# Kernel optimization log

Hardware: AMD Instinct MI355X
Metric: run time of the kernel (lower is better)

Reference implementation:

```python
import jax, jax.numpy as jnp
import numpy as np

B, S, D, H, DK, DV, DFF, L, V = 8, 1024, 256, 8, 32, 32, 1024, 4, 28
EPS = 1e-5
NEG = -1e9


def _ln(x, w, b):
    m = jnp.mean(x, axis=-1, keepdims=True)
    v = jnp.var(x, axis=-1, keepdims=True)
    return (x - m) * jax.lax.rsqrt(v + EPS) * w + b


def setup_inputs() -> dict:
    key = jax.random.key(0)
    ks = jax.random.split(key, 30)
    std = 0.02
    inp = {
        'input_ids': jax.random.randint(ks[0], (B, S), 0, V),
        'tok_embed': jax.random.normal(ks[1], (V, D), jnp.float32) * std,
        'pos_embed': jax.random.normal(ks[2], (S, D), jnp.float32) * std,
        'emb_ln_w': jnp.ones((D,), jnp.float32),
        'emb_ln_b': jnp.zeros((D,), jnp.float32),
        'Wq': jax.random.normal(ks[3], (L, D, H * DK), jnp.float32) * std,
        'bq': jnp.zeros((L, H * DK), jnp.float32),
        'Wk': jax.random.normal(ks[4], (L, D, H * DK), jnp.float32) * std,
        'bk': jnp.zeros((L, H * DK), jnp.float32),
        'Wv': jax.random.normal(ks[5], (L, D, H * DV), jnp.float32) * std,
        'bv': jnp.zeros((L, H * DV), jnp.float32),
        'Wo': jax.random.normal(ks[6], (L, H * DV, D), jnp.float32) * std,
        'bo': jnp.zeros((L, D), jnp.float32),
        'ln_w': jnp.ones((L, D), jnp.float32),
        'ln_b': jnp.zeros((L, D), jnp.float32),
        'W1': jax.random.normal(ks[7], (L, D, DFF), jnp.float32) * std,
        'b1': jnp.zeros((L, DFF), jnp.float32),
        'W2': jax.random.normal(ks[8], (L, DFF, D), jnp.float32) * std,
        'b2': jnp.zeros((L, D), jnp.float32),
        'ft1_w': jax.random.normal(ks[9], (D, D), jnp.float32) * std,
        'ft1_b': jnp.zeros((D,), jnp.float32),
        'ft2_w': jax.random.normal(ks[10], (D, D // 2), jnp.float32) * std,
        'ft2_b': jnp.zeros((D // 2,), jnp.float32),
        'cls_w': jax.random.normal(ks[11], (D // 2, 2), jnp.float32) * std,
        'cls_b': jnp.zeros((2,), jnp.float32),
    }
    return inp


def reference(input_ids, tok_embed, pos_embed, emb_ln_w, emb_ln_b,
              Wq, bq, Wk, bk, Wv, bv, Wo, bo, ln_w, ln_b,
              W1, b1, W2, b2, ft1_w, ft1_b, ft2_w, ft2_b, cls_w, cls_b):
    # Embedding: tok + pos, then LayerNorm
    x = tok_embed[input_ids] + pos_embed[jnp.arange(S)][None, :, :]
    x = _ln(x, emb_ln_w, emb_ln_b)
    # pad mask: True where key position is pad (token id 0); broadcast [B,1,1,S]
    pad = (input_ids == 0)[:, None, None, :]
    scale = 1.0 / np.sqrt(DK)
    for i in range(L):
        residual = x
        q = (x @ Wq[i] + bq[i]).reshape(B, S, H, DK).transpose(0, 2, 1, 3)
        k = (x @ Wk[i] + bk[i]).reshape(B, S, H, DK).transpose(0, 2, 1, 3)
        v = (x @ Wv[i] + bv[i]).reshape(B, S, H, DV).transpose(0, 2, 1, 3)
        scores = jnp.einsum('bhqd,bhkd->bhqk', q, k) * scale
        scores = jnp.where(pad, NEG, scores)
        attn = jax.nn.softmax(scores, axis=-1)
        ctx = jnp.einsum('bhqk,bhkd->bhqd', attn, v)
        ctx = ctx.transpose(0, 2, 1, 3).reshape(B, S, H * DV)
        x = _ln(ctx @ Wo[i] + bo[i] + residual, ln_w[i], ln_b[i])
        # FFN (note: original has NO residual/norm after FFN)
        x = jax.nn.relu(x @ W1[i] + b1[i]) @ W2[i] + b2[i]
    cls = x[:, 0, :]
    feat = jax.nn.relu(cls @ ft1_w + ft1_b) @ ft2_w + ft2_b  # dropout = eval no-op
    logits = feat @ cls_w + cls_b
    return logits, feat
```

## Files before the change

### kernel.cpp

```cpp
#include <hip/hip_runtime.h>
#include <math.h>

#define S_ 1024
#define D_ 256

typedef __attribute__((ext_vector_type(8))) _Float16 half8;
typedef __attribute__((ext_vector_type(4))) _Float16 half4;
typedef __attribute__((ext_vector_type(4))) float f32x4;
typedef __attribute__((ext_vector_type(4))) unsigned int u32x4;

__device__ __forceinline__ float wave_sum64(float x) {
    x += __shfl_xor(x, 32); x += __shfl_xor(x, 16); x += __shfl_xor(x, 8);
    x += __shfl_xor(x, 4);  x += __shfl_xor(x, 2);  x += __shfl_xor(x, 1);
    return x;
}

__device__ __forceinline__ unsigned int pk2h(float lo, float hi) {
    unsigned short a = __builtin_bit_cast(unsigned short, (_Float16)lo);
    unsigned short b = __builtin_bit_cast(unsigned short, (_Float16)hi);
    return (unsigned int)a | ((unsigned int)b << 16);
}

#define GLD16(gp, lp) __builtin_amdgcn_global_load_lds( \
    (const __attribute__((address_space(1))) void*)(gp), \
    (__attribute__((address_space(3))) void*)(lp), 16, 0, 0)

__global__ __launch_bounds__(256) void transpose_cvt(
    const float* __restrict__ src, _Float16* __restrict__ dst, int K, int N)
{
    __shared__ float tile[32][33];
    src += (size_t)blockIdx.z * K * N;
    dst += (size_t)blockIdx.z * K * N;
    const int bx = blockIdx.x * 32;
    const int by = blockIdx.y * 32;
    const int t = threadIdx.x;
    const int c = t & 31, r0 = t >> 5;
    #pragma unroll
    for (int j = 0; j < 4; ++j)
        tile[r0 + 8 * j][c] = src[(size_t)(by + r0 + 8 * j) * N + bx + c];
    __syncthreads();
    #pragma unroll
    for (int j = 0; j < 4; ++j)
        dst[(size_t)(bx + r0 + 8 * j) * K + by + c] = (_Float16)tile[c][r0 + 8 * j];
}

__global__ __launch_bounds__(256) void transpose_qkv(
    const float* __restrict__ Wq, const float* __restrict__ Wk,
    const float* __restrict__ Wv, _Float16* __restrict__ qkvT)
{
    __shared__ float tile[32][33];
    const int z = blockIdx.z, l = z / 3, m = z % 3;
    const float* src = (m == 0 ? Wq : (m == 1 ? Wk : Wv)) + (size_t)l * 65536;
    _Float16* dst = qkvT + (size_t)l * 196608 + (size_t)m * 65536;
    const int bx = blockIdx.x * 32;
    const int by = blockIdx.y * 32;
    const int t = threadIdx.x;
    const int c = t & 31, r0 = t >> 5;
    #pragma unroll
    for (int j = 0; j < 4; ++j)
        tile[r0 + 8 * j][c] = src[(size_t)(by + r0 + 8 * j) * 256 + bx + c];
    __syncthreads();
    #pragma unroll
    for (int j = 0; j < 4; ++j)
        dst[(size_t)(bx + r0 + 8 * j) * 256 + by + c] = (_Float16)tile[c][r0 + 8 * j];
}

__global__ __launch_bounds__(256) void pack_bias(
    const float* __restrict__ bq, const float* __restrict__ bk,
    const float* __restrict__ bv, float* __restrict__ bqkv)
{
    const int z = blockIdx.x, l = z / 3, m = z % 3;
    const float* s = (m == 0 ? bq : (m == 1 ? bk : bv)) + l * 256;
    bqkv[l * 768 + m * 256 + threadIdx.x] = s[threadIdx.x];
}

__global__ __launch_bounds__(64) void embed_ln_kernel(
    const int* __restrict__ ids, const float* __restrict__ tok,
    const float* __restrict__ pos, const float* __restrict__ w,
    const float* __restrict__ b, float* __restrict__ X, _Float16* __restrict__ Xh)
{
    const int tokid = blockIdx.x;
    const int s = tokid & (S_ - 1);
    const int t = threadIdx.x;
    const int id = ids[tokid];
    float4 e = *(const float4*)&tok[id * D_ + t * 4];
    float4 p = *(const float4*)&pos[s * D_ + t * 4];
    float4 x = make_float4(e.x + p.x, e.y + p.y, e.z + p.z, e.w + p.w);
    float sum = x.x + x.y + x.z + x.w;
    float sq  = x.x * x.x + x.y * x.y + x.z * x.z + x.w * x.w;
    sum = wave_sum64(sum); sq = wave_sum64(sq);
    float mean = sum * (1.f / D_);
    float var  = sq * (1.f / D_) - mean * mean;
    float rs   = rsqrtf(var + 1e-5f);
    float4 wv = *(const float4*)&w[t * 4];
    float4 bv = *(const float4*)&b[t * 4];
    float4 o = make_float4((x.x - mean) * rs * wv.x + bv.x,
                           (x.y - mean) * rs * wv.y + bv.y,
                           (x.z - mean) * rs * wv.z + bv.z,
                           (x.w - mean) * rs * wv.w + bv.w);
    *(float4*)&X[(size_t)tokid * D_ + t * 4] = o;
    half4 oh = { (_Float16)o.x, (_Float16)o.y, (_Float16)o.z, (_Float16)o.w };
    *(half4*)&Xh[(size_t)tokid * D_ + t * 4] = oh;
}

__global__ __launch_bounds__(64) void ln_res_kernel(
    const float* __restrict__ Y, const float* __restrict__ R,
    const float* __restrict__ w, const float* __restrict__ b,
    _Float16* __restrict__ Th)
{
    const int tokid = blockIdx.x;
    const int t = threadIdx.x;
    const size_t base = (size_t)tokid * D_ + t * 4;
    float4 y = *(const float4*)&Y[base];
    float4 r = *(const float4*)&R[base];
    float4 x = make_float4(y.x + r.x, y.y + r.y, y.z + r.z, y.w + r.w);
    float sum = x.x + x.y + x.z + x.w;
    float sq  = x.x * x.x + x.y * x.y + x.z * x.z + x.w * x.w;
    sum = wave_sum64(sum); sq = wave_sum64(sq);
    float mean = sum * (1.f / D_);
    float var  = sq * (1.f / D_) - mean * mean;
    float rs   = rsqrtf(var + 1e-5f);
    float4 wv = *(const float4*)&w[t * 4];
    float4 bv = *(const float4*)&b[t * 4];
    half4 oh = { (_Float16)((x.x - mean) * rs * wv.x + bv.x),
                 (_Float16)((x.y - mean) * rs * wv.y + bv.y),
                 (_Float16)((x.z - mean) * rs * wv.z + bv.z),
                 (_Float16)((x.w - mean) * rs * wv.w + bv.w) };
    *(half4*)&Th[base] = oh;
}

template<int MODE>
__global__ __launch_bounds__(256) void gemm_f16(
    const _Float16* __restrict__ A, const _Float16* __restrict__ Bt,
    const float* __restrict__ bias,
    float* __restrict__ Cf, _Float16* __restrict__ Ch,
    int K, int N)
{
    __shared__ _Float16 As[2][8192];
    const int t = threadIdx.x;
    const int wid = t >> 6, lane = t & 63;
    const int wr = wid >> 1, wc = wid & 1;
    const int m0 = blockIdx.x * 128, n0 = blockIdx.y * 64;
    const int li = lane & 15, lg = lane >> 4;
    const int srow = lane >> 3;
    const int scg = (lane & 7) ^ srow;

    f32x4 acc[4][2];
    const f32x4 zf = {0.f, 0.f, 0.f, 0.f};
    #pragma unroll
    for (int mr = 0; mr < 4; ++mr) { acc[mr][0] = zf; acc[mr][1] = zf; }

    const int KT = K >> 6;
    {
        const _Float16* Ab = A + (size_t)m0 * K;
        #pragma unroll
        for (int j = 0; j < 4; ++j) {
            int row = (wid * 4 + j) * 8 + srow;
            GLD16(Ab + (size_t)row * K + scg * 8, &As[0][(wid * 4 + j) * 512]);
        }
    }
    __syncthreads();

    for (int kt = 0; kt < KT; ++kt) {
        const int cur = kt & 1;
        if (kt + 1 < KT) {
            const _Float16* Ab = A + (size_t)m0 * K + (kt + 1) * 64;
            #pragma unroll
            for (int j = 0; j < 4; ++j) {
                int row = (wid * 4 + j) * 8 + srow;
                GLD16(Ab + (size_t)row * K + scg * 8, &As[cur ^ 1][(wid * 4 + j) * 512]);
            }
        }
        half8 bfr[2][2];
        #pragma unroll
        for (int nr = 0; nr < 2; ++nr) {
            const _Float16* bp = Bt + (size_t)(n0 + wc * 32 + nr * 16 + li) * K + kt * 64 + lg * 8;
            bfr[nr][0] = *(const half8*)bp;
            bfr[nr][1] = *(const half8*)(bp + 32);
        }
        #pragma unroll
        for (int kk = 0; kk < 2; ++kk) {
            half8 af[4];
            #pragma unroll
            for (int mr = 0; mr < 4; ++mr) {
                int arow = wr * 64 + mr * 16 + li;
                int ablk = (kk * 4 + lg) ^ (li & 7);
                af[mr] = *(const half8*)&As[cur][arow * 64 + ablk * 8];
            }
            #pragma unroll
            for (int mr = 0; mr < 4; ++mr)
                #pragma unroll
                for (int nr = 0; nr < 2; ++nr)
                    acc[mr][nr] = __builtin_amdgcn_mfma_f32_16x16x32_f16(
                        af[mr], bfr[nr][kk], acc[mr][nr], 0, 0, 0);
        }
        __syncthreads();
    }

    #pragma unroll
    for (int nr = 0; nr < 2; ++nr) {
        const int n = n0 + wc * 32 + nr * 16 + li;
        const float bv = bias[n];
        #pragma unroll
        for (int mr = 0; mr < 4; ++mr) {
            #pragma unroll
            for (int r = 0; r < 4; ++r) {
                const int m = m0 + wr * 64 + mr * 16 + lg * 4 + r;
                float o = acc[mr][nr][r] + bv;
                if (MODE == 1) o = fmaxf(o, 0.f);
                if (MODE == 0 || MODE == 2) Cf[(size_t)m * N + n] = o;
                if (MODE != 0) Ch[(size_t)m * N + n] = (_Float16)o;
            }
        }
    }
}

__global__ __launch_bounds__(256, 4) void attn_f16_kernel(
    const _Float16* __restrict__ qkv, const int* __restrict__ ids,
    _Float16* __restrict__ ctxo)
{
    __shared__ unsigned int Vp[32 * 36];
    __shared__ float maskn[64];
    const int t = threadIdx.x;
    const int bh = blockIdx.x, b = bh >> 3, h = bh & 7;
    const int q0 = blockIdx.y * 64;
    const int wid = t >> 6;
    const int lane = t & 63;
    const int i = lane & 15;
    const int g = lane >> 4;
    const int kp = t >> 3;
    const int v0s = (t & 7) * 4;

    const size_t bS = (size_t)b * S_;
    const float scale = 0.17677669529663687f;

    const half8 qf = *(const half8*)(qkv + (bS + q0 + wid * 16 + i) * 768 + h * 32 + g * 8);

    float m = -INFINITY, l = 0.f;
    f32x4 cacc[2];
    const f32x4 zf = {0.f, 0.f, 0.f, 0.f};
    cacc[0] = zf; cacc[1] = zf;

    const _Float16* kbase = qkv + 256 + (bS + i) * 768 + h * 32 + g * 8;
    const _Float16* vbase = qkv + 512 + (bS + 2 * kp) * 768 + h * 32 + v0s;

    for (int kt = 0; kt < 16; ++kt) {
        const int k0 = kt * 64;
        {
            const ushort* vb = (const ushort*)(vbase + (size_t)k0 * 768);
            ushort4 a0 = *(const ushort4*)vb;
            ushort4 a1 = *(const ushort4*)(vb + 768);
            u32x4 wv;
            wv[0] = (unsigned)a0.x | ((unsigned)a1.x << 16);
            wv[1] = (unsigned)a0.y | ((unsigned)a1.y << 16);
            wv[2] = (unsigned)a0.z | ((unsigned)a1.z << 16);
            wv[3] = (unsigned)a0.w | ((unsigned)a1.w << 16);
            *(u32x4*)&Vp[kp * 36 + v0s] = wv;
            if (t < 64) maskn[t] = (ids[bS + k0 + t] == 0) ? -1e9f : 0.f;
        }
        half8 kf[4];
        const _Float16* kb = kbase + (size_t)k0 * 768;
        #pragma unroll
        for (int c = 0; c < 4; ++c) kf[c] = *(const half8*)(kb + c * 16 * 768);
        f32x4 sacc[4];
        #pragma unroll
        for (int c = 0; c < 4; ++c)
            sacc[c] = __builtin_amdgcn_mfma_f32_16x16x32_f16(kf[c], qf, zf, 0, 0, 0);
        __syncthreads();
        float p[4][4];
        float tmax = -INFINITY;
        #pragma unroll
        for (int c = 0; c < 4; ++c) {
            float4 ad = *(const float4*)&maskn[c * 16 + g * 4];
            p[c][0] = fmaf(sacc[c][0], scale, ad.x);
            p[c][1] = fmaf(sacc[c][1], scale, ad.y);
            p[c][2] = fmaf(sacc[c][2], scale, ad.z);
            p[c][3] = fmaf(sacc[c][3], scale, ad.w);
            tmax = fmaxf(tmax, fmaxf(fmaxf(p[c][0], p[c][1]), fmaxf(p[c][2], p[c][3])));
        }
        tmax = fmaxf(tmax, __shfl_xor(tmax, 16));
        tmax = fmaxf(tmax, __shfl_xor(tmax, 32));
        float mn  = fmaxf(m, tmax);
        float fac = __expf(m - mn);
        float psum = 0.f;
        #pragma unroll
        for (int c = 0; c < 4; ++c) {
            p[c][0] = __expf(p[c][0] - mn); p[c][1] = __expf(p[c][1] - mn);
            p[c][2] = __expf(p[c][2] - mn); p[c][3] = __expf(p[c][3] - mn);
            psum += (p[c][0] + p[c][1]) + (p[c][2] + p[c][3]);
        }
        psum += __shfl_xor(psum, 16);
        psum += __shfl_xor(psum, 32);
        l = l * fac + psum;
        m = mn;
        cacc[0] *= fac;
        cacc[1] *= fac;
        unsigned int wrd[4][2];
        #pragma unroll
        for (int c = 0; c < 4; ++c) {
            wrd[c][0] = pk2h(p[c][0], p[c][1]);
            wrd[c][1] = pk2h(p[c][2], p[c][3]);
        }
        #pragma unroll
        for (int kc = 0; kc < 2; ++kc) {
            u32x4 bw;
            #pragma unroll
            for (int j2 = 0; j2 < 4; ++j2) {
                int src = ((2 * (g & 1) + (j2 >> 1)) << 4) + i;
                unsigned int lo = (unsigned int)__shfl((int)wrd[2 * kc][j2 & 1], src);
                unsigned int hi = (unsigned int)__shfl((int)wrd[2 * kc + 1][j2 & 1], src);
                bw[j2] = (g >= 2) ? hi : lo;
            }
            half8 pf = __builtin_bit_cast(half8, bw);
            #pragma unroll
            for (int vh = 0; vh < 2; ++vh) {
                const unsigned int* vp = &Vp[(kc * 16 + g * 4) * 36 + vh * 16 + i];
                u32x4 vw;
                vw[0] = vp[0]; vw[1] = vp[36]; vw[2] = vp[72]; vw[3] = vp[108];
                half8 vf = __builtin_bit_cast(half8, vw);
                cacc[vh] = __builtin_amdgcn_mfma_f32_16x16x32_f16(vf, pf, cacc[vh], 0, 0, 0);
            }
        }
        __syncthreads();
    }
    const float inv = 1.f / l;
    _Float16* crow = ctxo + (bS + q0 + wid * 16 + i) * 256 + h * 32;
    #pragma unroll
    for (int vh = 0; vh < 2; ++vh) {
        half4 st;
        #pragma unroll
        for (int r = 0; r < 4; ++r) st[r] = (_Float16)(cacc[vh][r] * inv);
        *(half4*)&crow[vh * 16 + g * 4] = st;
    }
}

__global__ __launch_bounds__(256) void head_kernel(
    const float* __restrict__ X,
    const float* __restrict__ ft1w, const float* __restrict__ ft1b,
    const float* __restrict__ ft2w, const float* __restrict__ ft2b,
    const float* __restrict__ clw,  const float* __restrict__ clb,
    float* __restrict__ out)
{
    __shared__ float clsS[8][256];
    __shared__ float h1S[8][256];
    __shared__ float featS[8][128];
    const int t = threadIdx.x;
    #pragma unroll
    for (int j = 0; j < 8; ++j) {
        int idx = t + j * 256;
        int b = idx >> 8, d = idx & 255;
        clsS[b][d] = X[(size_t)b * S_ * D_ + d];
    }
    __syncthreads();
    {
        float s[8] = {};
        for (int d = 0; d < 256; ++d) {
            float w = ft1w[d * 256 + t];
            #pragma unroll
            for (int b = 0; b < 8; ++b) s[b] = fmaf(clsS[b][d], w, s[b]);
        }
        float bias = ft1b[t];
        #pragma unroll
        for (int b = 0; b < 8; ++b) h1S[b][t] = fmaxf(s[b] + bias, 0.f);
    }
    __syncthreads();
    #pragma unroll
    for (int j = 0; j < 4; ++j) {
        int idx = t + j * 256;
        int b = idx >> 7, c = idx & 127;
        float s = 0.f;
        for (int d = 0; d < 256; ++d) s = fmaf(h1S[b][d], ft2w[d * 128 + c], s);
        s += ft2b[c];
        featS[b][c] = s;
        out[16 + idx] = s;
    }
    __syncthreads();
    if (t < 16) {
        int b = t >> 1, c = t & 1;
        float s = 0.f;
        for (int d = 0; d < 128; ++d) s = fmaf(featS[b][d], clw[d * 2 + c], s);
        out[t] = s + clb[c];
    }
}

extern "C" void kernel_launch(void* const* d_in, const int* in_sizes, int n_in,
                              void* d_out, int out_size, void* d_ws, size_t ws_size,
                              hipStream_t stream)
{
    const int*   ids  = (const int*)d_in[0];
    const float* tok  = (const float*)d_in[1];
    const float* pos  = (const float*)d_in[2];
    const float* elnw = (const float*)d_in[3];
    const float* elnb = (const float*)d_in[4];
    const float* Wq   = (const float*)d_in[5];
    const float* bq   = (const float*)d_in[6];
    const float* Wk   = (const float*)d_in[7];
    const float* bk   = (const float*)d_in[8];
    const float* Wv   = (const float*)d_in[9];
    const float* bv   = (const float*)d_in[10];
    const float* Wo   = (const float*)d_in[11];
    const float* bo   = (const float*)d_in[12];
    const float* lnw  = (const float*)d_in[13];
    const float* lnb  = (const float*)d_in[14];
    const float* W1   = (const float*)d_in[15];
    const float* b1   = (const float*)d_in[16];
    const float* W2   = (const float*)d_in[17];
    const float* b2   = (const float*)d_in[18];
    const float* ft1w = (const float*)d_in[19];
    const float* ft1b = (const float*)d_in[20];
    const float* ft2w = (const float*)d_in[21];
    const float* ft2b = (const float*)d_in[22];
    const float* clw  = (const float*)d_in[23];
    const float* clb  = (const float*)d_in[24];
    float* out = (float*)d_out;

    char* ws = (char*)d_ws;
    float*    X    = (float*)(ws);
    float*    Y    = (float*)(ws + (8ull << 20));
    _Float16* Xh   = (_Float16*)(ws + (16ull << 20));
    _Float16* Th   = (_Float16*)(ws + (20ull << 20));
    _Float16* qkvb = (_Float16*)(ws + (24ull << 20));
    _Float16* ctx  = (_Float16*)(ws + (36ull << 20));
    _Float16* Hb   = (_Float16*)(ws + (24ull << 20));
    _Float16* qkvT = (_Float16*)(ws + (40ull << 20));
    _Float16* WoT  = (_Float16*)(ws + (42ull << 20));
    _Float16* W1T  = (_Float16*)(ws + (43ull << 20));
    _Float16* W2T  = (_Float16*)(ws + (45ull << 20));
    float*    bqkv = (float*)(ws + (47ull << 20));

    transpose_qkv<<<dim3(8, 8, 12), 256, 0, stream>>>(Wq, Wk, Wv, qkvT);
    transpose_cvt<<<dim3(8, 8, 4),  256, 0, stream>>>(Wo, WoT, 256, 256);
    transpose_cvt<<<dim3(32, 8, 4), 256, 0, stream>>>(W1, W1T, 256, 1024);
    transpose_cvt<<<dim3(8, 32, 4), 256, 0, stream>>>(W2, W2T, 1024, 256);
    pack_bias<<<12, 256, 0, stream>>>(bq, bk, bv, bqkv);

    embed_ln_kernel<<<8192, 64, 0, stream>>>(ids, tok, pos, elnw, elnb, X, Xh);

    for (int i = 0; i < 4; ++i) {
        gemm_f16<3><<<dim3(64, 12), 256, 0, stream>>>(
            Xh, qkvT + (size_t)i * 196608, bqkv + i * 768, nullptr, qkvb, 256, 768);
        attn_f16_kernel<<<dim3(64, 16), 256, 0, stream>>>(qkvb, ids, ctx);
        gemm_f16<0><<<dim3(64, 4), 256, 0, stream>>>(
            ctx, WoT + (size_t)i * 65536, bo + i * 256, Y, nullptr, 256, 256);
        ln_res_kernel<<<8192, 64, 0, stream>>>(Y, X, lnw + i * 256, lnb + i * 256, Th);
        gemm_f16<1><<<dim3(64, 16), 256, 0, stream>>>(
            Th, W1T + (size_t)i * 262144, b1 + i * 1024, nullptr, Hb, 256, 1024);
        gemm_f16<2><<<dim3(64, 4), 256, 0, stream>>>(
            Hb, W2T + (size_t)i * 262144, b2 + i * 256, X, Xh, 1024, 256);
    }

    head_kernel<<<1, 256, 0, stream>>>(X, ft1w, ft1b, ft2w, ft2b, clw, clb, out);
}
```

Measured before the change: 477.9 us.

## Fuse residual into Wo GEMM, pack LN rows, relax GEMM sync, parallelize head

The residual add moves into the Wo-projection GEMM epilogue (new MODE 4), so the LayerNorm kernel reads only one input. The embed and LN kernels now process four tokens per 256-thread block instead of one per 64-thread block. In the GEMM, the B-fragment loads are issued before the A prefetch, and __syncthreads is replaced by explicit vmcnt waits plus raw barriers. The single-block head is split into three kernels spread over several blocks, which adds launches in exchange for more parallelism. The hand-tuned vmcnt counts depend on instruction ordering and could be wrong if the compiler reorders loads.

New measurement: 441.6 us. -7.6%, faster.

```diff
diff --git a/kernel.cpp b/kernel.cpp
--- a/kernel.cpp
+++ b/kernel.cpp
@@ -74,17 +74,17 @@
     bqkv[l * 768 + m * 256 + threadIdx.x] = s[threadIdx.x];
 }
 
-__global__ __launch_bounds__(64) void embed_ln_kernel(
+__global__ __launch_bounds__(256) void embed_ln_kernel(
     const int* __restrict__ ids, const float* __restrict__ tok,
     const float* __restrict__ pos, const float* __restrict__ w,
     const float* __restrict__ b, float* __restrict__ X, _Float16* __restrict__ Xh)
 {
-    const int tokid = blockIdx.x;
+    const int wv_ = threadIdx.x >> 6, lane = threadIdx.x & 63;
+    const int tokid = blockIdx.x * 4 + wv_;
     const int s = tokid & (S_ - 1);
-    const int t = threadIdx.x;
     const int id = ids[tokid];
-    float4 e = *(const float4*)&tok[id * D_ + t * 4];
-    float4 p = *(const float4*)&pos[s * D_ + t * 4];
+    float4 e = *(const float4*)&tok[id * D_ + lane * 4];
+    float4 p = *(const float4*)&pos[s * D_ + lane * 4];
     float4 x = make_float4(e.x + p.x, e.y + p.y, e.z + p.z, e.w + p.w);
     float sum = x.x + x.y + x.z + x.w;
     float sq  = x.x * x.x + x.y * x.y + x.z * x.z + x.w * x.w;
@@ -92,36 +92,33 @@
     float mean = sum * (1.f / D_);
     float var  = sq * (1.f / D_) - mean * mean;
     float rs   = rsqrtf(var + 1e-5f);
-    float4 wv = *(const float4*)&w[t * 4];
-    float4 bv = *(const float4*)&b[t * 4];
+    float4 wv = *(const float4*)&w[lane * 4];
+    float4 bv = *(const float4*)&b[lane * 4];
     float4 o = make_float4((x.x - mean) * rs * wv.x + bv.x,
                            (x.y - mean) * rs * wv.y + bv.y,
                            (x.z - mean) * rs * wv.z + bv.z,
                            (x.w - mean) * rs * wv.w + bv.w);
-    *(float4*)&X[(size_t)tokid * D_ + t * 4] = o;
+    *(float4*)&X[(size_t)tokid * D_ + lane * 4] = o;
     half4 oh = { (_Float16)o.x, (_Float16)o.y, (_Float16)o.z, (_Float16)o.w };
-    *(half4*)&Xh[(size_t)tokid * D_ + t * 4] = oh;
-}
-
-__global__ __launch_bounds__(64) void ln_res_kernel(
-    const float* __restrict__ Y, const float* __restrict__ R,
-    const float* __restrict__ w, const float* __restrict__ b,
-    _Float16* __restrict__ Th)
-{
-    const int tokid = blockIdx.x;
-    const int t = threadIdx.x;
-    const size_t base = (size_t)tokid * D_ + t * 4;
-    float4 y = *(const float4*)&Y[base];
-    float4 r = *(const float4*)&R[base];
-    float4 x = make_float4(y.x + r.x, y.y + r.y, y.z + r.z, y.w + r.w);
+    *(half4*)&Xh[(size_t)tokid * D_ + lane * 4] = oh;
+}
+
+__global__ __launch_bounds__(256) void ln_kernel(
+    const float* __restrict__ Y, const float* __restrict__ w,
+    const float* __restrict__ b, _Float16* __restrict__ Th)
+{
+    const int wv_ = threadIdx.x >> 6, lane = threadIdx.x & 63;
+    const int tokid = blockIdx.x * 4 + wv_;
+    const size_t base = (size_t)tokid * D_ + lane * 4;
+    float4 x = *(const float4*)&Y[base];
     float sum = x.x + x.y + x.z + x.w;
     float sq  = x.x * x.x + x.y * x.y + x.z * x.z + x.w * x.w;
     sum = wave_sum64(sum); sq = wave_sum64(sq);
     float mean = sum * (1.f / D_);
     float var  = sq * (1.f / D_) - mean * mean;
     float rs   = rsqrtf(var + 1e-5f);
-    float4 wv = *(const float4*)&w[t * 4];
-    float4 bv = *(const float4*)&b[t * 4];
+    float4 wv = *(const float4*)&w[lane * 4];
+    float4 bv = *(const float4*)&b[lane * 4];
     half4 oh = { (_Float16)((x.x - mean) * rs * wv.x + bv.x),
                  (_Float16)((x.y - mean) * rs * wv.y + bv.y),
                  (_Float16)((x.z - mean) * rs * wv.z + bv.z),
@@ -132,7 +129,7 @@
 template<int MODE>
 __global__ __launch_bounds__(256) void gemm_f16(
     const _Float16* __restrict__ A, const _Float16* __restrict__ Bt,
-    const float* __restrict__ bias,
+    const float* __restrict__ bias, const float* __restrict__ res,
     float* __restrict__ Cf, _Float16* __restrict__ Ch,
     int K, int N)
 {
@@ -159,10 +156,16 @@
             GLD16(Ab + (size_t)row * K + scg * 8, &As[0][(wid * 4 + j) * 512]);
         }
     }
-    __syncthreads();
 
     for (int kt = 0; kt < KT; ++kt) {
         const int cur = kt & 1;
+        half8 bfr[2][2];
+        #pragma unroll
+        for (int nr = 0; nr < 2; ++nr) {
+            const _Float16* bp = Bt + (size_t)(n0 + wc * 32 + nr * 16 + li) * K + kt * 64 + lg * 8;
+            bfr[nr][0] = *(const half8*)bp;
+            bfr[nr][1] = *(const half8*)(bp + 32);
+        }
         if (kt + 1 < KT) {
             const _Float16* Ab = A + (size_t)m0 * K + (kt + 1) * 64;
             #pragma unroll
@@ -170,14 +173,11 @@
                 int row = (wid * 4 + j) * 8 + srow;
                 GLD16(Ab + (size_t)row * K + scg * 8, &As[cur ^ 1][(wid * 4 + j) * 512]);
             }
-        }
-        half8 bfr[2][2];
-        #pragma unroll
-        for (int nr = 0; nr < 2; ++nr) {
-            const _Float16* bp = Bt + (size_t)(n0 + wc * 32 + nr * 16 + li) * K + kt * 64 + lg * 8;
-            bfr[nr][0] = *(const half8*)bp;
-            bfr[nr][1] = *(const half8*)(bp + 32);
-        }
+            asm volatile("s_waitcnt vmcnt(8)" ::: "memory");
+        } else {
+            asm volatile("s_waitcnt vmcnt(4)" ::: "memory");
+        }
+        __builtin_amdgcn_s_barrier();
         #pragma unroll
         for (int kk = 0; kk < 2; ++kk) {
             half8 af[4];
@@ -194,7 +194,7 @@
                     acc[mr][nr] = __builtin_amdgcn_mfma_f32_16x16x32_f16(
                         af[mr], bfr[nr][kk], acc[mr][nr], 0, 0, 0);
         }
-        __syncthreads();
+        __builtin_amdgcn_s_barrier();
     }
 
     #pragma unroll
@@ -208,8 +208,9 @@
                 const int m = m0 + wr * 64 + mr * 16 + lg * 4 + r;
                 float o = acc[mr][nr][r] + bv;
                 if (MODE == 1) o = fmaxf(o, 0.f);
-                if (MODE == 0 || MODE == 2) Cf[(size_t)m * N + n] = o;
-                if (MODE != 0) Ch[(size_t)m * N + n] = (_Float16)o;
+                if (MODE == 4) o += res[(size_t)m * N + n];
+                if (MODE == 0 || MODE == 2 || MODE == 4) Cf[(size_t)m * N + n] = o;
+                if (MODE == 1 || MODE == 2 || MODE == 3) Ch[(size_t)m * N + n] = (_Float16)o;
             }
         }
     }
@@ -317,8 +318,8 @@
                 const unsigned int* vp = &Vp[(kc * 16 + g * 4) * 36 + vh * 16 + i];
                 u32x4 vw;
                 vw[0] = vp[0]; vw[1] = vp[36]; vw[2] = vp[72]; vw[3] = vp[108];
-                half8 vf = __builtin_bit_cast(half8, vw);
-                cacc[vh] = __builtin_amdgcn_mfma_f32_16x16x32_f16(vf, pf, cacc[vh], 0, 0, 0);
+                half8 vfh = __builtin_bit_cast(half8, vw);
+                cacc[vh] = __builtin_amdgcn_mfma_f32_16x16x32_f16(vfh, pf, cacc[vh], 0, 0, 0);
             }
         }
         __syncthreads();
@@ -334,51 +335,82 @@
     }
 }
 
-__global__ __launch_bounds__(256) void head_kernel(
-    const float* __restrict__ X,
-    const float* __restrict__ ft1w, const float* __restrict__ ft1b,
-    const float* __restrict__ ft2w, const float* __restrict__ ft2b,
-    const float* __restrict__ clw,  const float* __restrict__ clb,
+__global__ __launch_bounds__(256) void head1_kernel(
+    const float* __restrict__ X, const float* __restrict__ ft1w,
+    const float* __restrict__ ft1b, float* __restrict__ h1)
+{
+    __shared__ float clsS[8][256];
+    __shared__ float ps[8][8][32];
+    const int t = threadIdx.x;
+    #pragma unroll
+    for (int b = 0; b < 8; ++b) clsS[b][t] = X[(size_t)b * S_ * D_ + t];
+    __syncthreads();
+    const int n = t & 31, dg = t >> 5;
+    const int gn = blockIdx.x * 32 + n;
+    float s[8] = {};
+    for (int dd = 0; dd < 32; ++dd) {
+        int d = dg * 32 + dd;
+        float w = ft1w[d * 256 + gn];
+        #pragma unroll
+        for (int b = 0; b < 8; ++b) s[b] = fmaf(clsS[b][d], w, s[b]);
+    }
+    #pragma unroll
+    for (int b = 0; b < 8; ++b) ps[dg][b][n] = s[b];
+    __syncthreads();
+    {
+        const int b = t >> 5, nn = t & 31;
+        float a = 0.f;
+        #pragma unroll
+        for (int g = 0; g < 8; ++g) a += ps[g][b][nn];
+        const int gn2 = blockIdx.x * 32 + nn;
+        h1[b * 256 + gn2] = fmaxf(a + ft1b[gn2], 0.f);
+    }
+}
+
+__global__ __launch_bounds__(256) void head2_kernel(
+    const float* __restrict__ h1, const float* __restrict__ ft2w,
+    const float* __restrict__ ft2b, float* __restrict__ featW,
     float* __restrict__ out)
 {
-    __shared__ float clsS[8][256];
-    __shared__ float h1S[8][256];
-    __shared__ float featS[8][128];
-    const int t = threadIdx.x;
-    #pragma unroll
-    for (int j = 0; j < 8; ++j) {
-        int idx = t + j * 256;
-        int b = idx >> 8, d = idx & 255;
-        clsS[b][d] = X[(size_t)b * S_ * D_ + d];
-    }
+    __shared__ float hS[8][256];
+    __shared__ float ps[8][8][32];
+    const int t = threadIdx.x;
+    #pragma unroll
+    for (int b = 0; b < 8; ++b) hS[b][t] = h1[b * 256 + t];
+    __syncthreads();
+    const int n = t & 31, dg = t >> 5;
+    const int gn = blockIdx.x * 32 + n;
+    float s[8] = {};
+    for (int dd = 0; dd < 32; ++dd) {
+        int d = dg * 32 + dd;
+        float w = ft2w[d * 128 + gn];
+        #pragma unroll
+        for (int b = 0; b < 8; ++b) s[b] = fmaf(hS[b][d], w, s[b]);
+    }
+    #pragma unroll
+    for (int b = 0; b < 8; ++b) ps[dg][b][n] = s[b];
     __syncthreads();
     {
-        float s[8] = {};
-        for (int d = 0; d < 256; ++d) {
-            float w = ft1w[d * 256 + t];
-            #pragma unroll
-            for (int b = 0; b < 8; ++b) s[b] = fmaf(clsS[b][d], w, s[b]);
-        }
-        float bias = ft1b[t];
-        #pragma unroll
-        for (int b = 0; b < 8; ++b) h1S[b][t] = fmaxf(s[b] + bias, 0.f);
-    }
-    __syncthreads();
-    #pragma unroll
-    for (int j = 0; j < 4; ++j) {
-        int idx = t + j * 256;
-        int b = idx >> 7, c = idx & 127;
+        const int b = t >> 5, nn = t & 31;
+        float a = 0.f;
+        #pragma unroll
+        for (int g = 0; g < 8; ++g) a += ps[g][b][nn];
+        const int gn2 = blockIdx.x * 32 + nn;
+        float v = a + ft2b[gn2];
+        featW[b * 128 + gn2] = v;
+        out[16 + b * 128 + gn2] = v;
+    }
+}
+
+__global__ __launch_bounds__(64) void head3_kernel(
+    const float* __restrict__ featW, const float* __restrict__ clw,
+    const float* __restrict__ clb, float* __restrict__ out)
+{
+    const int t = threadIdx.x;
+    if (t < 16) {
+        const int b = t >> 1, c = t & 1;
         float s = 0.f;
-        for (int d = 0; d < 256; ++d) s = fmaf(h1S[b][d], ft2w[d * 128 + c], s);
-        s += ft2b[c];
-        featS[b][c] = s;
-        out[16 + idx] = s;
-    }
-    __syncthreads();
-    if (t < 16) {
-        int b = t >> 1, c = t & 1;
-        float s = 0.f;
-        for (int d = 0; d < 128; ++d) s = fmaf(featS[b][d], clw[d * 2 + c], s);
+        for (int d = 0; d < 128; ++d) s = fmaf(featW[b * 128 + d], clw[d * 2 + c], s);
         out[t] = s + clb[c];
     }
 }
@@ -427,6 +459,8 @@
     _Float16* W1T  = (_Float16*)(ws + (43ull << 20));
     _Float16* W2T  = (_Float16*)(ws + (45ull << 20));
     float*    bqkv = (float*)(ws + (47ull << 20));
+    float*    h1W  = (float*)(ws + (47ull << 20) + (16ull << 10));
+    float*    feW  = (float*)(ws + (47ull << 20) + (24ull << 10));
 
     transpose_qkv<<<dim3(8, 8, 12), 256, 0, stream>>>(Wq, Wk, Wv, qkvT);
     transpose_cvt<<<dim3(8, 8, 4),  256, 0, stream>>>(Wo, WoT, 256, 256);
@@ -434,20 +468,22 @@
     transpose_cvt<<<dim3(8, 32, 4), 256, 0, stream>>>(W2, W2T, 1024, 256);
     pack_bias<<<12, 256, 0, stream>>>(bq, bk, bv, bqkv);
 
-    embed_ln_kernel<<<8192, 64, 0, stream>>>(ids, tok, pos, elnw, elnb, X, Xh);
+    embed_ln_kernel<<<2048, 256, 0, stream>>>(ids, tok, pos, elnw, elnb, X, Xh);
 
     for (int i = 0; i < 4; ++i) {
         gemm_f16<3><<<dim3(64, 12), 256, 0, stream>>>(
-            Xh, qkvT + (size_t)i * 196608, bqkv + i * 768, nullptr, qkvb, 256, 768);
+            Xh, qkvT + (size_t)i * 196608, bqkv + i * 768, nullptr, nullptr, qkvb, 256, 768);
         attn_f16_kernel<<<dim3(64, 16), 256, 0, stream>>>(qkvb, ids, ctx);
-        gemm_f16<0><<<dim3(64, 4), 256, 0, stream>>>(
-            ctx, WoT + (size_t)i * 65536, bo + i * 256, Y, nullptr, 256, 256);
-        ln_res_kernel<<<8192, 64, 0, stream>>>(Y, X, lnw + i * 256, lnb + i * 256, Th);
+        gemm_f16<4><<<dim3(64, 4), 256, 0, stream>>>(
+            ctx, WoT + (size_t)i * 65536, bo + i * 256, X, Y, nullptr, 256, 256);
+        ln_kernel<<<2048, 256, 0, stream>>>(Y, lnw + i * 256, lnb + i * 256, Th);
         gemm_f16<1><<<dim3(64, 16), 256, 0, stream>>>(
-            Th, W1T + (size_t)i * 262144, b1 + i * 1024, nullptr, Hb, 256, 1024);
+            Th, W1T + (size_t)i * 262144, b1 + i * 1024, nullptr, nullptr, Hb, 256, 1024);
         gemm_f16<2><<<dim3(64, 4), 256, 0, stream>>>(
-            Hb, W2T + (size_t)i * 262144, b2 + i * 256, X, Xh, 1024, 256);
-    }
-
-    head_kernel<<<1, 256, 0, stream>>>(X, ft1w, ft1b, ft2w, ft2b, clw, clb, out);
-}
+            Hb, W2T + (size_t)i * 262144, b2 + i * 256, nullptr, X, Xh, 1024, 256);
+    }
+
+    head1_kernel<<<8, 256, 0, stream>>>(X, ft1w, ft1b, h1W);
+    head2_kernel<<<4, 256, 0, stream>>>(h1W, ft2w, ft2b, feW, out);
+    head3_kernel<<<1, 64, 0, stream>>>(feW, clw, clb, out);
+}
```
